# Kernel optimization log

Hardware: AMD Instinct MI355X
Metric: run time of the kernel (lower is better)

The kernel has to match this reference:

```python
import jax, jax.numpy as jnp
import numpy as np

B, T, C = 4, 2048, 2048
H, N = 32, 64  # heads, head_size
EPS = 1e-5


def setup_inputs() -> dict:
    key = jax.random.key(0)
    ks = jax.random.split(key, 16)
    s = 0.02
    return {
        'hidden': jax.random.normal(ks[0], (B, T, C), jnp.float32),
        'time_decay': jax.random.normal(ks[1], (H, N), jnp.float32),
        'time_first': jax.random.normal(ks[2], (H, N), jnp.float32),
        'Wr': jax.random.normal(ks[3], (C, C), jnp.float32) * s,
        'Wk': jax.random.normal(ks[4], (C, C), jnp.float32) * s,
        'Wv': jax.random.normal(ks[5], (C, C), jnp.float32) * s,
        'Wg': jax.random.normal(ks[6], (C, C), jnp.float32) * s,
        'Wo': jax.random.normal(ks[7], (C, C), jnp.float32) * s,
        'mix_r': jax.random.uniform(ks[8], (1, 1, C), jnp.float32),
        'mix_k': jax.random.uniform(ks[9], (1, 1, C), jnp.float32),
        'mix_v': jax.random.uniform(ks[10], (1, 1, C), jnp.float32),
        'mix_g': jax.random.uniform(ks[11], (1, 1, C), jnp.float32),
        'ln_w': jax.random.uniform(ks[12], (C,), jnp.float32, 0.5, 1.5),
        'ln_b': jax.random.normal(ks[13], (C,), jnp.float32) * 0.1,
        'init_state': jnp.zeros((B, H, N, N), jnp.float32),
    }


def reference(hidden, time_decay, time_first, Wr, Wk, Wv, Wg, Wo,
              mix_r, mix_k, mix_v, mix_g, ln_w, ln_b, init_state):
    b, t, c = hidden.shape
    h, n = time_decay.shape
    # time shift: shifted[:, 0] = 0 (fresh state), shifted[:, i] = hidden[:, i-1]
    shifted = jnp.pad(hidden, ((0, 0), (1, 0), (0, 0)))[:, :-1]
    xk = hidden * mix_k + shifted * (1.0 - mix_k)
    xv = hidden * mix_v + shifted * (1.0 - mix_v)
    xr = hidden * mix_r + shifted * (1.0 - mix_r)
    xg = hidden * mix_g + shifted * (1.0 - mix_g)

    r = (xr @ Wr).astype(jnp.float32).reshape(b, t, h, n)
    k = (xk @ Wk).astype(jnp.float32).reshape(b, t, h, n)
    v = (xv @ Wv).astype(jnp.float32).reshape(b, t, h, n)
    gate = jax.nn.silu(xg @ Wg)  # [b,t,c]

    w = jnp.exp(-jnp.exp(time_decay.astype(jnp.float32)))  # [h,n] decay per k-channel
    u = time_first.astype(jnp.float32)                      # [h,n]

    def step(state, rkv):
        rt, kt, vt = rkv  # each [b,h,n]
        at = kt[..., :, None] * vt[..., None, :]  # outer product kt @ vt -> [b,h,n,n]
        out_t = jnp.einsum('bhn,bhnm->bhm', rt, u[None, :, :, None] * at + state)
        new_state = at + w[None, :, :, None] * state
        return new_state, out_t

    rT = jnp.moveaxis(r, 1, 0)  # [t,b,h,n]
    kT = jnp.moveaxis(k, 1, 0)
    vT = jnp.moveaxis(v, 1, 0)
    final_state, outT = jax.lax.scan(step, init_state.astype(jnp.float32), (rT, kT, vT))
    out = jnp.moveaxis(outT, 0, 1)  # [b,t,h,n]

    # GroupNorm with num_groups = h over the c = h*n channels
    mean = out.mean(-1, keepdims=True)
    var = out.var(-1, keepdims=True)
    out = (out - mean) / jnp.sqrt(var + EPS)
    out = out.reshape(b, t, c) * ln_w + ln_b

    out = out.astype(hidden.dtype) * gate
    out = out @ Wo
    return out, final_state
```

## Files before the change

### kernel.cpp

```cpp
#include <hip/hip_runtime.h>
#include <stdint.h>

typedef unsigned short ushort_t;
typedef __attribute__((ext_vector_type(8))) short bf16x8;
typedef __attribute__((ext_vector_type(4))) float f32x4;
typedef __attribute__((ext_vector_type(8))) unsigned short u16x8;

__device__ __forceinline__ ushort_t f2bf(float f) {
  union { float f; unsigned u; } v; v.f = f;
  unsigned r = v.u + 0x7fffu + ((v.u >> 16) & 1u);
  return (ushort_t)(r >> 16);
}
__device__ __forceinline__ float bf2f(ushort_t u) {
  union { unsigned u; float f; } v; v.u = ((unsigned)u) << 16;
  return v.f;
}

__device__ __forceinline__ void gload_lds16(const void* g, void* l) {
  __builtin_amdgcn_global_load_lds(
      (const __attribute__((address_space(1))) void*)g,
      (__attribute__((address_space(3))) void*)l, 16, 0, 0);
}

struct PrepArgs {
  const float* W[5];
  ushort_t* Wt[5];
  const float* Hd;
  const float* mr; const float* mk; const float* mv; const float* mg;
  ushort_t* xr; ushort_t* xk; ushort_t* xv; ushort_t* xg;
};

__global__ __launch_bounds__(256) void prep(PrepArgs a, int n, int Mrows, int Tt) {
  const int z = blockIdx.z;
  if (z < 5) {
    const float* __restrict__ W = a.W[z];
    ushort_t* __restrict__ Wt = a.Wt[z];
    __shared__ float tile[32][33];
    const int tx = threadIdx.x & 31, ty = threadIdx.x >> 5;
    const int bx = blockIdx.x, by = blockIdx.y;
#pragma unroll
    for (int r = 0; r < 4; ++r)
      tile[ty + 8 * r][tx] = W[(size_t)(by * 32 + ty + 8 * r) * n + bx * 32 + tx];
    __syncthreads();
#pragma unroll
    for (int r = 0; r < 4; ++r)
      Wt[(size_t)(bx * 32 + ty + 8 * r) * n + by * 32 + tx] =
          f2bf(tile[tx][ty + 8 * r]);
    return;
  }
  const int Cc = n;
  const float* __restrict__ Hd = a.Hd;
  const size_t n8 = (size_t)Mrows * Cc / 8;
  const int bid = blockIdx.y * gridDim.x + blockIdx.x;
  for (size_t idx = (size_t)bid * blockDim.x + threadIdx.x; idx < n8;
       idx += (size_t)gridDim.x * gridDim.y * blockDim.x) {
    const size_t e = idx * 8;
    const int m = (int)(e / (size_t)Cc);
    const int c = (int)(e % (size_t)Cc);
    const int t = m % Tt;
    f32x4 h0 = *(const f32x4*)&Hd[e];
    f32x4 h1 = *(const f32x4*)&Hd[e + 4];
    f32x4 sA = {0.f, 0.f, 0.f, 0.f}, sB = {0.f, 0.f, 0.f, 0.f};
    if (t != 0) {
      sA = *(const f32x4*)&Hd[e - Cc];
      sB = *(const f32x4*)&Hd[e - Cc + 4];
    }
    f32x4 mA[4], mB[4];
    mA[0] = *(const f32x4*)&a.mr[c]; mB[0] = *(const f32x4*)&a.mr[c + 4];
    mA[1] = *(const f32x4*)&a.mk[c]; mB[1] = *(const f32x4*)&a.mk[c + 4];
    mA[2] = *(const f32x4*)&a.mv[c]; mB[2] = *(const f32x4*)&a.mv[c + 4];
    mA[3] = *(const f32x4*)&a.mg[c]; mB[3] = *(const f32x4*)&a.mg[c + 4];
    u16x8 o[4];
#pragma unroll
    for (int w = 0; w < 4; ++w) {
#pragma unroll
      for (int q = 0; q < 4; ++q) {
        o[w][q]     = f2bf(sA[q] + (h0[q] - sA[q]) * mA[w][q]);
        o[w][q + 4] = f2bf(sB[q] + (h1[q] - sB[q]) * mB[w][q]);
      }
    }
    *(u16x8*)&a.xr[e] = o[0];
    *(u16x8*)&a.xk[e] = o[1];
    *(u16x8*)&a.xv[e] = o[2];
    *(u16x8*)&a.xg[e] = o[3];
  }
}

struct GemmArgs {
  const ushort_t* A[4];
  const ushort_t* Bt[4];
  void* C[4];
};

__device__ __forceinline__ void stage_mat(const ushort_t* __restrict__ base,
                                          int K, int voff, char* ldsmat,
                                          int tid) {
#pragma unroll
  for (int hf = 0; hf < 2; ++hf)
#pragma unroll
    for (int s = 0; s < 2; ++s)
      gload_lds16(base + (size_t)(hf * 128 + s * 64) * K + voff,
                  ldsmat + hf * 16384 + s * 8192 + tid * 16);
}

template <int BF16OUT>
__global__ __launch_bounds__(512, 1) void gemm256(GemmArgs args, int M, int N, int K) {
  extern __shared__ char lds[];
  const int z = blockIdx.z;
  const ushort_t* __restrict__ A = args.A[z];
  const ushort_t* __restrict__ Bt = args.Bt[z];

  const int tid = threadIdx.x;
  const int lane = tid & 63, w = tid >> 6;
  const int wm = w >> 2, wn = w & 3;
  const int r16 = lane & 15, kb = lane >> 4;

  const int nbx = N >> 8;
  const int nwg = nbx * (M >> 8);
  const int orig = blockIdx.y * nbx + blockIdx.x;
  const int wid = (orig & 7) * (nwg >> 3) + (orig >> 3);
  const int bm0 = (wid / nbx) << 8;
  const int bn0 = (wid % nbx) << 8;

  const int trow = tid >> 3;
  const int voff = trow * K + (((((tid & 7) * 16) ^ ((trow & 7) << 4))) >> 1);
  const ushort_t* __restrict__ Abase = A + (size_t)bm0 * K;
  const ushort_t* __restrict__ Bbase = Bt + (size_t)bn0 * K;

  int aoff[8], boff[4];
#pragma unroll
  for (int mi = 0; mi < 8; ++mi) {
    const int d = (mi * 16 + r16) * 128 + kb * 16;
    aoff[mi] = wm * 16384 + (d ^ (((d >> 7) & 7) << 4));
  }
#pragma unroll
  for (int ni = 0; ni < 4; ++ni) {
    const int d = ((wn & 1) * 64 + ni * 16 + r16) * 128 + kb * 16;
    boff[ni] = 32768 + (wn >> 1) * 16384 + (d ^ (((d >> 7) & 7) << 4));
  }

  f32x4 acc[8][4] = {};
  const int NT = K >> 6;

  stage_mat(Abase, K, voff, lds, tid);
  stage_mat(Bbase, K, voff, lds + 32768, tid);
  stage_mat(Abase + 64, K, voff, lds + 65536, tid);
  stage_mat(Bbase + 64, K, voff, lds + 65536 + 32768, tid);
  asm volatile("s_waitcnt vmcnt(8)" ::: "memory");
  asm volatile("s_barrier" ::: "memory");

  for (int t = 0; t < NT; ++t) {
    const int cur = t & 1;
    char* cbase = lds + cur * 65536;
    bf16x8 ah[4][2], bq[4][2];

#pragma unroll
    for (int m = 0; m < 4; ++m) {
      ah[m][0] = *(const bf16x8*)(cbase + aoff[m]);
      ah[m][1] = *(const bf16x8*)(cbase + (aoff[m] ^ 64));
    }
#pragma unroll
    for (int n = 0; n < 2; ++n) {
      bq[n][0] = *(const bf16x8*)(cbase + boff[n]);
      bq[n][1] = *(const bf16x8*)(cbase + (boff[n] ^ 64));
    }
    asm volatile("s_barrier" ::: "memory");
    __builtin_amdgcn_s_setprio(1);
#pragma unroll
    for (int m = 0; m < 4; ++m)
#pragma unroll
      for (int n = 0; n < 2; ++n)
#pragma unroll
        for (int ks = 0; ks < 2; ++ks)
          acc[m][n] = __builtin_amdgcn_mfma_f32_16x16x32_bf16(
              ah[m][ks], bq[n][ks], acc[m][n], 0, 0, 0);
    __builtin_amdgcn_s_setprio(0);

#pragma unroll
    for (int n = 2; n < 4; ++n) {
      bq[n][0] = *(const bf16x8*)(cbase + boff[n]);
      bq[n][1] = *(const bf16x8*)(cbase + (boff[n] ^ 64));
    }
    asm volatile("s_barrier" ::: "memory");
    __builtin_amdgcn_s_setprio(1);
#pragma unroll
    for (int m = 0; m < 4; ++m)
#pragma unroll
      for (int n = 2; n < 4; ++n)
#pragma unroll
        for (int ks = 0; ks < 2; ++ks)
          acc[m][n] = __builtin_amdgcn_mfma_f32_16x16x32_bf16(
              ah[m][ks], bq[n][ks], acc[m][n], 0, 0, 0);
    __builtin_amdgcn_s_setprio(0);

#pragma unroll
    for (int m = 0; m < 4; ++m) {
      ah[m][0] = *(const bf16x8*)(cbase + aoff[4 + m]);
      ah[m][1] = *(const bf16x8*)(cbase + (aoff[4 + m] ^ 64));
    }
    asm volatile("s_barrier" ::: "memory");
    if (t + 2 < NT)
      stage_mat(Abase + (t + 2) * 64, K, voff, cbase, tid);
    __builtin_amdgcn_s_setprio(1);
#pragma unroll
    for (int m = 0; m < 4; ++m)
#pragma unroll
      for (int n = 0; n < 2; ++n)
#pragma unroll
        for (int ks = 0; ks < 2; ++ks)
          acc[4 + m][n] = __builtin_amdgcn_mfma_f32_16x16x32_bf16(
              ah[m][ks], bq[n][ks], acc[4 + m][n], 0, 0, 0);

    if (t + 2 < NT)
      stage_mat(Bbase + (t + 2) * 64, K, voff, cbase + 32768, tid);
#pragma unroll
    for (int m = 0; m < 4; ++m)
#pragma unroll
      for (int n = 2; n < 4; ++n)
#pragma unroll
        for (int ks = 0; ks < 2; ++ks)
          acc[4 + m][n] = __builtin_amdgcn_mfma_f32_16x16x32_bf16(
              ah[m][ks], bq[n][ks], acc[4 + m][n], 0, 0, 0);
    __builtin_amdgcn_s_setprio(0);

    if (t + 1 < NT) {
      if (t + 2 < NT)
        asm volatile("s_waitcnt vmcnt(8)" ::: "memory");
      else
        asm volatile("s_waitcnt vmcnt(0)" ::: "memory");
      asm volatile("s_barrier" ::: "memory");
    }
  }

  const int row0 = bm0 + wm * 128 + kb * 4;
  const int col0 = bn0 + wn * 64 + r16;
#pragma unroll
  for (int mi = 0; mi < 8; ++mi)
#pragma unroll
    for (int ni = 0; ni < 4; ++ni) {
      f32x4 v = acc[mi][ni];
      const int row = row0 + mi * 16;
      const int col = col0 + ni * 16;
#pragma unroll
      for (int rr = 0; rr < 4; ++rr) {
        if (BF16OUT)
          ((ushort_t*)args.C[z])[(size_t)(row + rr) * N + col] = f2bf(v[rr]);
        else
          ((float*)args.C[z])[(size_t)(row + rr) * N + col] = v[rr];
      }
    }
}

__global__ __launch_bounds__(512, 1) void wkv_chunk(
    const ushort_t* __restrict__ Rm, const ushort_t* __restrict__ Km,
    const ushort_t* __restrict__ Vm, const float* __restrict__ td,
    const float* __restrict__ tf,
    float* __restrict__ Oatt, float* __restrict__ chunkA,
    int Tt, int Hh, int NC, int Lc) {
  extern __shared__ char smem[];
  ushort_t* Rs  = (ushort_t*)(smem + 0);
  ushort_t* Ks  = (ushort_t*)(smem + 18432);
  ushort_t* Ks2 = (ushort_t*)(smem + 36864);
  ushort_t* Vt  = (ushort_t*)(smem + 55296);
  ushort_t* Kt  = (ushort_t*)(smem + 72704);
  ushort_t* At  = (ushort_t*)(smem + 90112);
  float* wp   = (float*)(smem + 124928);
  float* w16p = (float*)(smem + 129280);
  float* u_   = (float*)(smem + 131456);

  const int blk = blockIdx.x;
  const int bh = blk / NC, c = blk % NC;
  const int b = bh / Hh, h = bh % Hh;
  const int tid = threadIdx.x;
  const int lane = tid & 63, w = tid >> 6;
  const int r16 = lane & 15, g = lane >> 4;
  const int Cc = Hh * 64;
  const size_t base = ((size_t)b * Tt + (size_t)c * Lc) * Cc + h * 64;

  const int srow = tid >> 2;
  const int scol = (tid & 3) * 16;
  const size_t gb = base + (size_t)srow * Cc + scol;
  u16x8 r0 = *(const u16x8*)&Rm[gb];
  u16x8 r1 = *(const u16x8*)&Rm[gb + 8];
  u16x8 k0 = *(const u16x8*)&Km[gb];
  u16x8 k1 = *(const u16x8*)&Km[gb + 8];
  u16x8 v0 = *(const u16x8*)&Vm[gb];
  u16x8 v1 = *(const u16x8*)&Vm[gb + 8];

  if (tid < 64) {
    const float ev = expf(td[h * 64 + tid]);
    const float wv = expf(-ev);
    u_[tid] = tf[h * 64 + tid];
    float p = 1.f;
#pragma unroll
    for (int d = 0; d < 16; ++d) { wp[d * 68 + tid] = p; p *= wv; }
    float pq = 1.f;
#pragma unroll
    for (int q = 0; q < 8; ++q) { w16p[q * 68 + tid] = pq; pq *= p; }
  }
  __syncthreads();

  {
    *(u16x8*)&Rs[srow * 72 + scol] = r0;
    *(u16x8*)&Rs[srow * 72 + scol + 8] = r1;
    *(u16x8*)&Ks[srow * 72 + scol] = k0;
    *(u16x8*)&Ks[srow * 72 + scol + 8] = k1;
    const int s16 = srow & 15, shi = srow >> 4;
    const float* fa = &wp[(15 - s16) * 68 + scol];
    const float* gq = &w16p[(7 - shi) * 68 + scol];
    u16x8 a2, b2;
#pragma unroll
    for (int e = 0; e < 8; ++e) {
      a2[e] = f2bf(bf2f(k0[e]) * fa[e]);
      b2[e] = f2bf(bf2f(k1[e]) * fa[e + 8]);
    }
    *(u16x8*)&Ks2[srow * 72 + scol] = a2;
    *(u16x8*)&Ks2[srow * 72 + scol + 8] = b2;
#pragma unroll
    for (int e = 0; e < 8; ++e) {
      Vt[(scol + e) * 136 + srow] = v0[e];
      Vt[(scol + 8 + e) * 136 + srow] = v1[e];
      Kt[(scol + e) * 136 + srow] = f2bf(bf2f(k0[e]) * fa[e] * gq[e]);
      Kt[(scol + 8 + e) * 136 + srow] =
          f2bf(bf2f(k1[e]) * fa[e + 8] * gq[e + 8]);
    }
    const u16x8 z = {};
    for (int o = tid; o < (128 * 136) / 8; o += 512) *(u16x8*)&At[o * 8] = z;
  }
  __syncthreads();

  for (int p = w; p < 28; p += 8) {
    int tau = 1, cum = 0;
    while (cum + tau <= p) { cum += tau; ++tau; }
    const int sig = p - cum;
    const float* wr  = &wp[r16 * 68];
    const float* w16 = &w16p[(tau - sig - 1) * 68];
    f32x4 acc = {0.f, 0.f, 0.f, 0.f};
#pragma unroll
    for (int ks = 0; ks < 2; ++ks) {
      const int ib = ks * 32 + g * 8;
      u16x8 rv = *(const u16x8*)&Rs[(tau * 16 + r16) * 72 + ib];
      bf16x8 kv = *(const bf16x8*)&Ks2[(sig * 16 + r16) * 72 + ib];
      f32x4 wa = *(const f32x4*)&wr[ib];
      f32x4 wb = *(const f32x4*)&wr[ib + 4];
      f32x4 sa = *(const f32x4*)&w16[ib];
      f32x4 sb = *(const f32x4*)&w16[ib + 4];
      union { bf16x8 v; ushort_t s[8]; } af;
#pragma unroll
      for (int e = 0; e < 4; ++e) {
        af.s[e]     = f2bf(bf2f(rv[e]) * (wa[e] * sa[e]));
        af.s[e + 4] = f2bf(bf2f(rv[e + 4]) * (wb[e] * sb[e]));
      }
      acc = __builtin_amdgcn_mfma_f32_16x16x32_bf16(af.v, kv, acc, 0, 0, 0);
    }
#pragma unroll
    for (int r = 0; r < 4; ++r)
      At[(tau * 16 + g * 4 + r) * 136 + sig * 16 + r16] = f2bf(acc[r]);
  }

  for (int rr = 0; rr < 3; ++rr) {
    const int eid = tid + rr * 512;
    if (eid >= 1088) break;
    const int tile = eid / 136;
    const int e2 = eid % 136;
    int t = 0, cum = 0;
    while (cum + t + 1 <= e2) { cum += t + 1; ++t; }
    const int s = e2 - cum;
    const ushort_t* rrow = &Rs[(tile * 16 + t) * 72];
    const ushort_t* krow = &Ks[(tile * 16 + s) * 72];
    const float* frow = (s < t) ? &wp[(t - s - 1) * 68] : u_;
    float acc = 0.f;
#pragma unroll
    for (int i0 = 0; i0 < 64; i0 += 8) {
      u16x8 rv = *(const u16x8*)&rrow[i0];
      u16x8 kv = *(const u16x8*)&krow[i0];
      f32x4 f0 = *(const f32x4*)&frow[i0];
      f32x4 f1 = *(const f32x4*)&frow[i0 + 4];
#pragma unroll
      for (int e = 0; e < 4; ++e) {
        acc = fmaf(bf2f(rv[e]), bf2f(kv[e]) * f0[e], acc);
        acc = fmaf(bf2f(rv[e + 4]), bf2f(kv[e + 4]) * f1[e], acc);
      }
    }
    At[(tile * 16 + t) * 136 + tile * 16 + s] = f2bf(acc);
  }
  __syncthreads();

  {
    const int nk = (w + 2) >> 1;
#pragma unroll
    for (int jt = 0; jt < 4; ++jt) {
      f32x4 acc = {0.f, 0.f, 0.f, 0.f};
      for (int kk = 0; kk < nk; ++kk) {
        bf16x8 af = *(const bf16x8*)&At[(w * 16 + r16) * 136 + kk * 32 + g * 8];
        bf16x8 bv = *(const bf16x8*)&Vt[(jt * 16 + r16) * 136 + kk * 32 + g * 8];
        acc = __builtin_amdgcn_mfma_f32_16x16x32_bf16(af, bv, acc, 0, 0, 0);
      }
#pragma unroll
      for (int r = 0; r < 4; ++r)
        Oatt[base + (size_t)(w * 16 + g * 4 + r) * Cc + jt * 16 + r16] = acc[r];
    }
  }

#pragma unroll
  for (int q = 0; q < 2; ++q) {
    const int T = w * 2 + q;
    const int it = T >> 2, jt = T & 3;
    f32x4 acc = {0.f, 0.f, 0.f, 0.f};
#pragma unroll
    for (int kk = 0; kk < 4; ++kk) {
      const int s0 = kk * 32 + g * 8;
      bf16x8 af = *(const bf16x8*)&Kt[(it * 16 + r16) * 136 + s0];
      bf16x8 bv = *(const bf16x8*)&Vt[(jt * 16 + r16) * 136 + s0];
      acc = __builtin_amdgcn_mfma_f32_16x16x32_bf16(af, bv, acc, 0, 0, 0);
    }
#pragma unroll
    for (int r = 0; r < 4; ++r)
      chunkA[(size_t)blk * 4096 + (it * 16 + g * 4 + r) * 64 + jt * 16 + r16] =
          acc[r];
  }
}

__global__ __launch_bounds__(256) void chunk_carry(
    const float* __restrict__ chunkA, const float* __restrict__ s0,
    const float* __restrict__ td,
    float* __restrict__ chunkS, float* __restrict__ Sout,
    int Hh, int NC, int Lc) {
  const int blk = blockIdx.x;
  const int bh = blk >> 2, q = blk & 3;
  const int h = bh % Hh;
  const int e4 = q * 1024 + threadIdx.x * 4;
  const int i = e4 >> 6;
  const float wL = expf(-(float)Lc * expf(td[h * 64 + i]));
  f32x4 S = *(const f32x4*)&s0[(size_t)bh * 4096 + e4];
  for (int c = 0; c < NC; ++c) {
    *(f32x4*)&chunkS[((size_t)bh * NC + c) * 4096 + e4] = S;
    f32x4 A = *(const f32x4*)&chunkA[((size_t)bh * NC + c) * 4096 + e4];
#pragma unroll
    for (int t = 0; t < 4; ++t) S[t] = fmaf(wL, S[t], A[t]);
  }
  *(f32x4*)&Sout[(size_t)bh * 4096 + e4] = S;
}

__global__ __launch_bounds__(256) void chunk_out(
    const float* __restrict__ OattIn, const float* __restrict__ chunkS,
    const ushort_t* __restrict__ Rm, const ushort_t* __restrict__ Gm,
    const float* __restrict__ td,
    const float* __restrict__ lnw, const float* __restrict__ lnb,
    ushort_t* __restrict__ Xo, int Tt, int Hh, int NC, int Lc) {
  __shared__ float rL[128 * 64];
  const int blk = blockIdx.x;
  const int bh = blk / NC, c = blk % NC;
  const int b = bh / Hh, h = bh % Hh;
  const int tid = threadIdx.x;
  const int Cc = Hh * 64;
  const size_t rowbase = (size_t)b * Tt + (size_t)c * Lc;

  {
    const int i0 = (tid & 7) * 8;
    const int tb = tid >> 3;
    float e8[8];
#pragma unroll
    for (int qq = 0; qq < 8; ++qq) e8[qq] = expf(td[h * 64 + i0 + qq]);
#pragma unroll
    for (int m = 0; m < 4; ++m) {
      const int tau = tb + 32 * m;
      u16x8 rv = *(const u16x8*)&Rm[(rowbase + tau) * Cc + h * 64 + i0];
#pragma unroll
      for (int qq = 0; qq < 8; ++qq)
        rL[tau * 64 + i0 + qq] = bf2f(rv[qq]) * expf(-(float)tau * e8[qq]);
    }
  }

  const int lane = tid & 63, wv = tid >> 6;
  float Sc[64];
  {
    const float* Sp = chunkS + (size_t)blk * 4096 + lane;
#pragma unroll
    for (int i = 0; i < 64; ++i) Sc[i] = Sp[i * 64];
  }
  const float lw = lnw[h * 64 + lane];
  const float lb = lnb[h * 64 + lane];
  __syncthreads();

  for (int k = 0; k < Lc / 4; ++k) {
    const int tau = wv + 4 * k;
    const size_t goff = (rowbase + tau) * Cc + h * 64 + lane;
    float ac0 = OattIn[goff], ac1 = 0.f;
#pragma unroll
    for (int i0 = 0; i0 < 64; i0 += 8) {
      f32x4 rv0 = *(const f32x4*)&rL[tau * 64 + i0];
      f32x4 rv1 = *(const f32x4*)&rL[tau * 64 + i0 + 4];
      ac0 = fmaf(rv0[0], Sc[i0], ac0);
      ac0 = fmaf(rv0[1], Sc[i0 + 1], ac0);
      ac0 = fmaf(rv0[2], Sc[i0 + 2], ac0);
      ac0 = fmaf(rv0[3], Sc[i0 + 3], ac0);
      ac1 = fmaf(rv1[0], Sc[i0 + 4], ac1);
      ac1 = fmaf(rv1[1], Sc[i0 + 5], ac1);
      ac1 = fmaf(rv1[2], Sc[i0 + 6], ac1);
      ac1 = fmaf(rv1[3], Sc[i0 + 7], ac1);
    }
    const float acc = ac0 + ac1;
    float s = acc, s2 = acc * acc;
#pragma unroll
    for (int m = 1; m < 64; m <<= 1) {
      s += __shfl_xor(s, m);
      s2 += __shfl_xor(s2, m);
    }
    const float mean = s * (1.f / 64.f);
    const float var = s2 * (1.f / 64.f) - mean * mean;
    const float inv = 1.f / sqrtf(var + 1e-5f);
    const float y = (acc - mean) * inv * lw + lb;
    const float gv = bf2f(Gm[goff]);
    const float gate = gv / (1.f + expf(-gv));
    Xo[goff] = f2bf(y * gate);
  }
}

extern "C" void kernel_launch(void* const* d_in, const int* in_sizes, int n_in,
                              void* d_out, int out_size, void* d_ws, size_t ws_size,
                              hipStream_t stream) {
  const int B = 4, T = 2048, Cc = 2048, H = 32;
  const int M = B * T;
  const int NC = 16, Lc = 128;

  const float* hidden = (const float*)d_in[0];
  const float* td     = (const float*)d_in[1];
  const float* tf     = (const float*)d_in[2];
  const float* Wr     = (const float*)d_in[3];
  const float* Wk     = (const float*)d_in[4];
  const float* Wv     = (const float*)d_in[5];
  const float* Wg     = (const float*)d_in[6];
  const float* Wo     = (const float*)d_in[7];
  const float* mix_r  = (const float*)d_in[8];
  const float* mix_k  = (const float*)d_in[9];
  const float* mix_v  = (const float*)d_in[10];
  const float* mix_g  = (const float*)d_in[11];
  const float* lnw    = (const float*)d_in[12];
  const float* lnb    = (const float*)d_in[13];
  const float* s0     = (const float*)d_in[14];

  const size_t SZ_WT = (size_t)Cc * Cc * 2;
  const size_t SZ_X  = (size_t)M * Cc * 2;
  const size_t NEED  = 5 * SZ_WT + 6 * SZ_X;

  if (ws_size < NEED) return;

  float* out  = (float*)d_out;
  float* sfin = (float*)d_out + (size_t)M * Cc;
  ushort_t* xg = (ushort_t*)d_out;
  ushort_t* gb = (ushort_t*)d_out + (size_t)M * Cc;

  char* ws = (char*)d_ws;
  ushort_t* wt[5];
  for (int z = 0; z < 5; ++z) wt[z] = (ushort_t*)(ws + z * SZ_WT);
  char* regX = ws + 5 * SZ_WT;
  char* regY = regX + 3 * SZ_X;
  ushort_t* xr = (ushort_t*)regX;
  ushort_t* xk = (ushort_t*)(regX + SZ_X);
  ushort_t* xv = (ushort_t*)(regX + 2 * SZ_X);
  ushort_t* rb = (ushort_t*)regY;
  ushort_t* kb = (ushort_t*)(regY + SZ_X);
  ushort_t* vb = (ushort_t*)(regY + 2 * SZ_X);
  float* oatt   = (float*)regX;
  float* chunkA = (float*)(regX + 2 * SZ_X);
  float* chunkS = (float*)(regY + SZ_X);
  ushort_t* xo  = (ushort_t*)(regY + 2 * SZ_X);

  {
    PrepArgs a;
    a.W[0] = Wr; a.W[1] = Wk; a.W[2] = Wv; a.W[3] = Wg; a.W[4] = Wo;
    for (int z = 0; z < 5; ++z) a.Wt[z] = wt[z];
    a.Hd = hidden;
    a.mr = mix_r; a.mk = mix_k; a.mv = mix_v; a.mg = mix_g;
    a.xr = xr; a.xk = xk; a.xv = xv; a.xg = xg;
    dim3 g(Cc / 32, Cc / 32, 6);
    prep<<<g, 256, 0, stream>>>(a, Cc, M, T);
  }

  {
    const ushort_t* As[4] = {xr, xk, xv, xg};
    void* Cs[4] = {rb, kb, vb, gb};
    for (int z = 0; z < 4; ++z) {
      GemmArgs a = {};
      a.A[0] = As[z]; a.Bt[0] = wt[z]; a.C[0] = Cs[z];
      dim3 g(Cc / 256, M / 256, 1);
      gemm256<1><<<g, 512, 131072, stream>>>(a, M, Cc, Cc);
    }
  }

  wkv_chunk<<<B * H * NC, 512, 131712, stream>>>(rb, kb, vb, td, tf, oatt,
                                                 chunkA, T, H, NC, Lc);
  chunk_carry<<<B * H * 4, 256, 0, stream>>>(chunkA, s0, td, chunkS, sfin,
                                             H, NC, Lc);
  chunk_out<<<B * H * NC, 256, 0, stream>>>(oatt, chunkS, rb, gb, td, lnw, lnb,
                                            xo, T, H, NC, Lc);

  {
    GemmArgs a = {};
    a.A[0] = xo; a.Bt[0] = wt[4]; a.C[0] = out;
    dim3 g(Cc / 256, M / 256, 1);
    gemm256<0><<<g, 512, 131072, stream>>>(a, M, Cc, Cc);
  }
}
```

Measured before the change: 585.2 us.

## Compute chunk_out inter-chunk term with bf16 MFMA and precomputed decay powers

Rewrites chunk_out to compute the r·S inter-chunk contribution with bf16 16x16x32 MFMA instead of scalar FMAs over a 64-register state copy. Decay powers are built once per block from a small table of w^d and w^(16q) products rather than per-element expf. The block grows to 512 threads and results are staged in LDS before the GroupNorm/gate epilogue. This trades fp32 accuracy on r and state for bf16 and adds more LDS use and syncs.

```diff
diff --git a/kernel.cpp b/kernel.cpp
--- a/kernel.cpp
+++ b/kernel.cpp
@@ -442,65 +442,90 @@
   *(f32x4*)&Sout[(size_t)bh * 4096 + e4] = S;
 }
 
-__global__ __launch_bounds__(256) void chunk_out(
+__global__ __launch_bounds__(512) void chunk_out(
     const float* __restrict__ OattIn, const float* __restrict__ chunkS,
     const ushort_t* __restrict__ Rm, const ushort_t* __restrict__ Gm,
     const float* __restrict__ td,
     const float* __restrict__ lnw, const float* __restrict__ lnb,
     ushort_t* __restrict__ Xo, int Tt, int Hh, int NC, int Lc) {
-  __shared__ float rL[128 * 64];
+  __shared__ ushort_t rLb[128 * 72];
+  __shared__ ushort_t St[64 * 72];
+  __shared__ float Ob[128 * 68];
+  __shared__ float wp[16 * 68];
+  __shared__ float w16p[8 * 68];
+
   const int blk = blockIdx.x;
   const int bh = blk / NC, c = blk % NC;
   const int b = bh / Hh, h = bh % Hh;
   const int tid = threadIdx.x;
+  const int lane = tid & 63, w = tid >> 6;
+  const int r16 = lane & 15, g = lane >> 4;
   const int Cc = Hh * 64;
   const size_t rowbase = (size_t)b * Tt + (size_t)c * Lc;
 
+  const int srow = tid >> 2;
+  const int scol = (tid & 3) * 16;
+  u16x8 r0 = *(const u16x8*)&Rm[(rowbase + srow) * Cc + h * 64 + scol];
+  u16x8 r1 = *(const u16x8*)&Rm[(rowbase + srow) * Cc + h * 64 + scol + 8];
+  const int jj = tid & 63, i0 = (tid >> 6) * 8;
+  float sv[8];
+#pragma unroll
+  for (int e = 0; e < 8; ++e)
+    sv[e] = chunkS[(size_t)blk * 4096 + (i0 + e) * 64 + jj];
+
+  if (tid < 64) {
+    const float ev = expf(td[h * 64 + tid]);
+    const float wv = expf(-ev);
+    float p = 1.f;
+#pragma unroll
+    for (int d = 0; d < 16; ++d) { wp[d * 68 + tid] = p; p *= wv; }
+    float pq = 1.f;
+#pragma unroll
+    for (int q = 0; q < 8; ++q) { w16p[q * 68 + tid] = pq; pq *= p; }
+  }
+  __syncthreads();
+
   {
-    const int i0 = (tid & 7) * 8;
-    const int tb = tid >> 3;
-    float e8[8];
-#pragma unroll
-    for (int qq = 0; qq < 8; ++qq) e8[qq] = expf(td[h * 64 + i0 + qq]);
-#pragma unroll
-    for (int m = 0; m < 4; ++m) {
-      const int tau = tb + 32 * m;
-      u16x8 rv = *(const u16x8*)&Rm[(rowbase + tau) * Cc + h * 64 + i0];
-#pragma unroll
-      for (int qq = 0; qq < 8; ++qq)
-        rL[tau * 64 + i0 + qq] = bf2f(rv[qq]) * expf(-(float)tau * e8[qq]);
-    }
-  }
-
-  const int lane = tid & 63, wv = tid >> 6;
-  float Sc[64];
-  {
-    const float* Sp = chunkS + (size_t)blk * 4096 + lane;
-#pragma unroll
-    for (int i = 0; i < 64; ++i) Sc[i] = Sp[i * 64];
-  }
+    const float* fa = &wp[(srow & 15) * 68 + scol];
+    const float* gq = &w16p[(srow >> 4) * 68 + scol];
+    u16x8 a2, b2;
+#pragma unroll
+    for (int e = 0; e < 8; ++e) {
+      a2[e] = f2bf(bf2f(r0[e]) * (fa[e] * gq[e]));
+      b2[e] = f2bf(bf2f(r1[e]) * (fa[e + 8] * gq[e + 8]));
+    }
+    *(u16x8*)&rLb[srow * 72 + scol] = a2;
+    *(u16x8*)&rLb[srow * 72 + scol + 8] = b2;
+#pragma unroll
+    for (int e = 0; e < 8; ++e) St[jj * 72 + i0 + e] = f2bf(sv[e]);
+  }
+  __syncthreads();
+
+#pragma unroll
+  for (int jt = 0; jt < 4; ++jt) {
+    f32x4 acc;
+    const int row0 = w * 16 + g * 4;
+#pragma unroll
+    for (int r = 0; r < 4; ++r)
+      acc[r] = OattIn[(rowbase + row0 + r) * Cc + h * 64 + jt * 16 + r16];
+#pragma unroll
+    for (int ks = 0; ks < 2; ++ks) {
+      bf16x8 af = *(const bf16x8*)&rLb[(w * 16 + r16) * 72 + ks * 32 + g * 8];
+      bf16x8 bv = *(const bf16x8*)&St[(jt * 16 + r16) * 72 + ks * 32 + g * 8];
+      acc = __builtin_amdgcn_mfma_f32_16x16x32_bf16(af, bv, acc, 0, 0, 0);
+    }
+#pragma unroll
+    for (int r = 0; r < 4; ++r)
+      Ob[(row0 + r) * 68 + jt * 16 + r16] = acc[r];
+  }
+  __syncthreads();
+
   const float lw = lnw[h * 64 + lane];
   const float lb = lnb[h * 64 + lane];
-  __syncthreads();
-
-  for (int k = 0; k < Lc / 4; ++k) {
-    const int tau = wv + 4 * k;
+  for (int k = 0; k < 16; ++k) {
+    const int tau = w + 8 * k;
     const size_t goff = (rowbase + tau) * Cc + h * 64 + lane;
-    float ac0 = OattIn[goff], ac1 = 0.f;
-#pragma unroll
-    for (int i0 = 0; i0 < 64; i0 += 8) {
-      f32x4 rv0 = *(const f32x4*)&rL[tau * 64 + i0];
-      f32x4 rv1 = *(const f32x4*)&rL[tau * 64 + i0 + 4];
-      ac0 = fmaf(rv0[0], Sc[i0], ac0);
-      ac0 = fmaf(rv0[1], Sc[i0 + 1], ac0);
-      ac0 = fmaf(rv0[2], Sc[i0 + 2], ac0);
-      ac0 = fmaf(rv0[3], Sc[i0 + 3], ac0);
-      ac1 = fmaf(rv1[0], Sc[i0 + 4], ac1);
-      ac1 = fmaf(rv1[1], Sc[i0 + 5], ac1);
-      ac1 = fmaf(rv1[2], Sc[i0 + 6], ac1);
-      ac1 = fmaf(rv1[3], Sc[i0 + 7], ac1);
-    }
-    const float acc = ac0 + ac1;
+    const float acc = Ob[tau * 68 + lane];
     float s = acc, s2 = acc * acc;
 #pragma unroll
     for (int m = 1; m < 64; m <<= 1) {
@@ -593,7 +618,7 @@
                                                  chunkA, T, H, NC, Lc);
   chunk_carry<<<B * H * 4, 256, 0, stream>>>(chunkA, s0, td, chunkS, sfin,
                                              H, NC, Lc);
-  chunk_out<<<B * H * NC, 256, 0, stream>>>(oatt, chunkS, rb, gb, td, lnw, lnb,
+  chunk_out<<<B * H * NC, 512, 0, stream>>>(oatt, chunkS, rb, gb, td, lnw, lnb,
                                             xo, T, H, NC, Lc);
 
   {
```

Result: faster. 545.2 us (-6.8%).
